# Optimization experiments

Measured on AMD Instinct MI355X. Metric: run time of the kernel, lower is better.

## Reference

```python
import jax, jax.numpy as jnp
import numpy as np

N_NODES = 50000
N_EDGES = 800000
IN_DIM = 64
HID = 64
OUT_DIM = 40
NEG_SLOPE = 0.2


def _gat_layer(x, src, dst, W, b, att, bias, n_nodes):
    # x: [N, Fin] -> lin -> [N, Fout]; heads = 1
    h = x @ W.T + b
    x_i = h[dst]                      # [E, F] target features
    x_j = h[src]                      # [E, F] source features
    # edge attention logits: cat([x_i, x_j]) @ att.T -> [E, 1]
    alpha = jnp.concatenate([x_i, x_j], axis=-1) @ att.T
    alpha = jax.nn.leaky_relu(alpha, NEG_SLOPE)
    # segment softmax over destination node (pyg_utils.softmax)
    amax = jax.ops.segment_max(alpha, dst, num_segments=n_nodes)
    e = jnp.exp(alpha - amax[dst])
    denom = jax.ops.segment_sum(e, dst, num_segments=n_nodes)
    alpha = e / (denom[dst] + 1e-16)
    # message = alpha * x_j, aggr='add' scatter to dst, then + bias
    out = jax.ops.segment_sum(x_j * alpha, dst, num_segments=n_nodes)
    return out + bias


def setup_inputs() -> dict:
    key = jax.random.key(0)
    ks = jax.random.split(key, 12)
    x = jax.random.normal(ks[0], (N_NODES, IN_DIM), dtype=jnp.float32)
    edge_index = jax.random.randint(ks[1], (2, N_EDGES), 0, N_NODES, dtype=jnp.int64)
    def glorot(k, shape):
        fan_in, fan_out = shape[1], shape[0]
        lim = float(np.sqrt(6.0 / (fan_in + fan_out)))
        return jax.random.uniform(k, shape, jnp.float32, -lim, lim)
    W1 = glorot(ks[2], (HID, IN_DIM))
    b1 = jnp.zeros((HID,), jnp.float32)
    att1 = glorot(ks[3], (1, 2 * HID))
    bias1 = jnp.zeros((HID,), jnp.float32)
    W2 = glorot(ks[4], (HID, HID))
    b2 = jnp.zeros((HID,), jnp.float32)
    att2 = glorot(ks[5], (1, 2 * HID))
    bias2 = jnp.zeros((HID,), jnp.float32)
    Wp1 = glorot(ks[6], (HID, HID))
    bp1 = jnp.zeros((HID,), jnp.float32)
    Wp2 = glorot(ks[7], (OUT_DIM, HID))
    bp2 = jnp.zeros((OUT_DIM,), jnp.float32)
    return {"x": x, "edge_index": edge_index,
            "W1": W1, "b1": b1, "att1": att1, "bias1": bias1,
            "W2": W2, "b2": b2, "att2": att2, "bias2": bias2,
            "Wp1": Wp1, "bp1": bp1, "Wp2": Wp2, "bp2": bp2}


def reference(x, edge_index, W1, b1, att1, bias1, W2, b2, att2, bias2,
              Wp1, bp1, Wp2, bp2):
    src, dst = edge_index[0], edge_index[1]
    n = x.shape[0]
    # layer 1 (GAT) + relu; dropout p=0 in eval -> identity
    h = jax.nn.relu(_gat_layer(x, src, dst, W1, b1, att1, bias1, n))
    # layer 2 (GAT) + relu
    h = jax.nn.relu(_gat_layer(h, src, dst, W2, b2, att2, bias2, n))
    # post-MP MLP + log_softmax over classes
    h = h @ Wp1.T + bp1
    logits = h @ Wp2.T + bp2
    return jax.nn.log_softmax(logits, axis=1)
```

## Files before the change

kernel.cpp:

```cpp
#include <hip/hip_runtime.h>
#include <hip/hip_fp16.h>
#include <math.h>

#define NN 50000
#define NE 800000
#define NEG 0.2f

#define NPB 128
#define CHK 6250
#define NBUK 98
#define LCAP 10240

typedef __attribute__((ext_vector_type(8))) short short8v;
typedef __attribute__((ext_vector_type(4))) float f32x4;

__device__ __forceinline__ float lrelu(float x){ return x > 0.f ? x : NEG * x; }

__device__ __forceinline__ float bcastf(float v, int l){
    return __uint_as_float(__builtin_amdgcn_readlane(__float_as_uint(v), l));
}
__device__ __forceinline__ int bcasti(int v, int l){
    return (int)__builtin_amdgcn_readlane((unsigned)v, l);
}
__device__ __forceinline__ short bf16t(float x){ return (short)(__float_as_uint(x) >> 16); }
__device__ __forceinline__ float bf16tof(short s){
    return __uint_as_float(((unsigned)(unsigned short)s) << 16);
}

__global__ __launch_bounds__(256) void k_cntA(const int* __restrict__ dst,
                                              int* __restrict__ counts){
    __shared__ int c[NBUK];
    int tid = threadIdx.x, blk = blockIdx.x;
    for (int i = tid; i < NBUK; i += 256) c[i] = 0;
    __syncthreads();
    int beg = blk * CHK, end = min(beg + CHK, NE);
    for (int i = beg + tid; i < end; i += 256) atomicAdd(&c[dst[i] >> 9], 1);
    __syncthreads();
    for (int i = tid; i < NBUK; i += 256) counts[i * NPB + blk] = c[i];
}

__global__ __launch_bounds__(1024) void k_scanB(int* __restrict__ counts,
                                                int* __restrict__ bbase){
    __shared__ int swave[16];
    int tid = threadIdx.x, lane = tid & 63, wid = tid >> 6;
    const int M = NBUK * NPB;
    int carry = 0;
    for (int base = 0; base < M; base += 1024){
        int i = base + tid;
        int v = (i < M) ? counts[i] : 0;
        int incl = v;
        #pragma unroll
        for (int off = 1; off < 64; off <<= 1){
            int t = __shfl_up(incl, off);
            if (lane >= off) incl += t;
        }
        if (lane == 63) swave[wid] = incl;
        __syncthreads();
        if (wid == 0){
            int sv = (lane < 16) ? swave[lane] : 0;
            #pragma unroll
            for (int off = 1; off < 16; off <<= 1){
                int t = __shfl_up(sv, off);
                if (lane >= off) sv += t;
            }
            if (lane < 16) swave[lane] = sv;
        }
        __syncthreads();
        int woff = wid ? swave[wid - 1] : 0;
        if (i < M) counts[i] = carry + woff + incl - v;
        carry += swave[15];
        __syncthreads();
    }
    for (int i = tid; i < NBUK; i += 1024) bbase[i] = counts[i * NPB];
    if (tid == 0) bbase[NBUK] = NE;
}

__global__ __launch_bounds__(256) void k_partC(const int* __restrict__ src,
                                               const int* __restrict__ dst,
                                               const int* __restrict__ cofs,
                                               unsigned* __restrict__ part){
    __shared__ int lcur[NBUK];
    int tid = threadIdx.x, blk = blockIdx.x;
    for (int i = tid; i < NBUK; i += 256) lcur[i] = cofs[i * NPB + blk];
    __syncthreads();
    int beg = blk * CHK, end = min(beg + CHK, NE);
    for (int i = beg + tid; i < end; i += 256){
        int d = dst[i];
        int pos = atomicAdd(&lcur[d >> 9], 1);
        part[pos] = ((unsigned)(d & 511) << 16) | (unsigned)src[i];
    }
}

__global__ __launch_bounds__(256) void k_buildD(const unsigned* __restrict__ part,
                                                const int* __restrict__ bbase,
                                                int* __restrict__ rowstart,
                                                int* __restrict__ csr){
    __shared__ int hist[512], cur[512];
    __shared__ int csrbuf[LCAP];
    __shared__ int swave[4];
    int tid = threadIdx.x, lane = tid & 63, wid = tid >> 6;
    int b = blockIdx.x;
    int ebeg = bbase[b], eend = bbase[b + 1], cnt = eend - ebeg;

    for (int i = tid; i < 512; i += 256) hist[i] = 0;
    __syncthreads();
    for (int i = tid; i < cnt; i += 256) atomicAdd(&hist[part[ebeg + i] >> 16], 1);
    __syncthreads();

    int h0 = hist[2 * tid], h1 = hist[2 * tid + 1];
    int v = h0 + h1, incl = v;
    #pragma unroll
    for (int off = 1; off < 64; off <<= 1){
        int t = __shfl_up(incl, off);
        if (lane >= off) incl += t;
    }
    if (lane == 63) swave[wid] = incl;
    __syncthreads();
    int woff = 0;
    #pragma unroll
    for (int w = 0; w < 4; ++w) if (w < wid) woff += swave[w];
    int e0 = woff + incl - v;
    int e1 = e0 + h0;
    cur[2 * tid] = e0; cur[2 * tid + 1] = e1;
    int gi = b * 512 + 2 * tid;
    if (gi     <= NN) rowstart[gi]     = ebeg + e0;
    if (gi + 1 <= NN) rowstart[gi + 1] = ebeg + e1;
    __syncthreads();

    for (int i = tid; i < cnt; i += 256){
        unsigned u = part[ebeg + i];
        int lp = atomicAdd(&cur[u >> 16], 1);
        if (lp < LCAP) csrbuf[lp] = (int)(u & 0xFFFFu);
    }
    __syncthreads();
    int m = min(cnt, LCAP);
    for (int i = tid; i < m; i += 256) csr[ebeg + i] = csrbuf[i];
}

__global__ __launch_bounds__(256) void k_lin_mfma(const float* __restrict__ X,
                                                  const float* __restrict__ W,
                                                  const float* __restrict__ b,
                                                  const float* __restrict__ att,
                                                  __half* __restrict__ Hh,
                                                  float* __restrict__ ad,
                                                  float* __restrict__ as_, int n){
    int lane = threadIdx.x & 63, wid = threadIdx.x >> 6;
    int nb = blockIdx.x * 64 + wid * 16;
    if (nb >= n) return;
    int r0 = lane & 15, rg = lane >> 4;

    short8v a_hi[2], a_lo[2];
    int arow = nb + r0; if (arow >= n) arow = n - 1;
    const float* xp = X + (size_t)arow * 64 + rg * 8;
    #pragma unroll
    for (int ks = 0; ks < 2; ++ks){
        #pragma unroll
        for (int j = 0; j < 8; ++j){
            float v = xp[ks * 32 + j];
            short h = bf16t(v);
            a_hi[ks][j] = h;
            a_lo[ks][j] = bf16t(v - bf16tof(h));
        }
    }

    f32x4 acc[4] = {{0,0,0,0},{0,0,0,0},{0,0,0,0},{0,0,0,0}};
    #pragma unroll
    for (int nt = 0; nt < 4; ++nt){
        const float* wp = W + (size_t)(nt * 16 + r0) * 64 + rg * 8;
        #pragma unroll
        for (int ks = 0; ks < 2; ++ks){
            short8v b_hi, b_lo;
            #pragma unroll
            for (int j = 0; j < 8; ++j){
                float v = wp[ks * 32 + j];
                short h = bf16t(v);
                b_hi[j] = h;
                b_lo[j] = bf16t(v - bf16tof(h));
            }
            acc[nt] = __builtin_amdgcn_mfma_f32_16x16x32_bf16(a_hi[ks], b_hi, acc[nt], 0, 0, 0);
            acc[nt] = __builtin_amdgcn_mfma_f32_16x16x32_bf16(a_hi[ks], b_lo, acc[nt], 0, 0, 0);
            acc[nt] = __builtin_amdgcn_mfma_f32_16x16x32_bf16(a_lo[ks], b_hi, acc[nt], 0, 0, 0);
        }
    }

    #pragma unroll
    for (int nt = 0; nt < 4; ++nt){
        float bb = b[nt * 16 + r0];
        #pragma unroll
        for (int q = 0; q < 4; ++q){
            int node = nb + rg * 4 + q;
            float v = acc[nt][q] + bb;
            acc[nt][q] = v;
            if (node < n) Hh[(size_t)node * 64 + nt * 16 + r0] = __float2half(v);
        }
    }

    float attd[4], atts[4];
    #pragma unroll
    for (int nt = 0; nt < 4; ++nt){
        attd[nt] = att[nt * 16 + r0];
        atts[nt] = att[64 + nt * 16 + r0];
    }
    #pragma unroll
    for (int q = 0; q < 4; ++q){
        float pd = 0.f, ps = 0.f;
        #pragma unroll
        for (int nt = 0; nt < 4; ++nt){
            pd = fmaf(attd[nt], acc[nt][q], pd);
            ps = fmaf(atts[nt], acc[nt][q], ps);
        }
        #pragma unroll
        for (int off = 8; off; off >>= 1){
            pd += __shfl_xor(pd, off);
            ps += __shfl_xor(ps, off);
        }
        int node = nb + rg * 4 + q;
        if (r0 == 0 && node < n){ ad[node] = pd; as_[node] = ps; }
    }
}

__global__ __launch_bounds__(256) void k_agg(const __half* __restrict__ Hh,
                                             const float* __restrict__ ad,
                                             const float* __restrict__ as_,
                                             const int* __restrict__ rowstart,
                                             const int* __restrict__ csr,
                                             const float* __restrict__ bias,
                                             float* __restrict__ OUT, int n){
    int tid = threadIdx.x, lane = tid & 63, wid = tid >> 6;
    int node = blockIdx.x * 4 + wid;
    if (node >= n) return;
    int beg = rowstart[node], end = rowstart[node + 1];
    float adn = ad[node];

    float acc = 0.f, denom = 0.f;
    for (int cbeg = beg; cbeg < end; cbeg += 64){
        int k = cbeg + lane;
        int s = (k < end) ? csr[k] : 0;
        float e = (k < end) ? __expf(lrelu(adn + as_[s])) : 0.f;
        float es = e;
        #pragma unroll
        for (int off = 32; off; off >>= 1) es += __shfl_xor(es, off);
        denom += es;
        int cnt = min(64, end - cbeg);
        int j = 0;
        for (; j + 4 <= cnt; j += 4){
            int   sa = bcasti(s, j),     sb = bcasti(s, j + 1);
            int   sc = bcasti(s, j + 2), sd = bcasti(s, j + 3);
            float ea = bcastf(e, j),     eb = bcastf(e, j + 1);
            float ec = bcastf(e, j + 2), ed = bcastf(e, j + 3);
            float ha = __half2float(Hh[(size_t)sa * 64 + lane]);
            float hb = __half2float(Hh[(size_t)sb * 64 + lane]);
            float hc = __half2float(Hh[(size_t)sc * 64 + lane]);
            float hd = __half2float(Hh[(size_t)sd * 64 + lane]);
            acc = fmaf(ea, ha, acc);
            acc = fmaf(eb, hb, acc);
            acc = fmaf(ec, hc, acc);
            acc = fmaf(ed, hd, acc);
        }
        for (; j < cnt; ++j){
            int   sj = bcasti(s, j);
            float ej = bcastf(e, j);
            acc = fmaf(ej, __half2float(Hh[(size_t)sj * 64 + lane]), acc);
        }
    }

    float o = acc / (denom + 1e-16f) + bias[lane];
    OUT[node * 64 + lane] = fmaxf(o, 0.f);
}

__global__ void k_wcomb(const float* __restrict__ Wp1, const float* __restrict__ bp1,
                        const float* __restrict__ Wp2, const float* __restrict__ bp2,
                        float* __restrict__ Wc, float* __restrict__ bc){
    int idx = blockIdx.x * 256 + threadIdx.x;
    if (idx < 40 * 64){
        int c = idx >> 6, k = idx & 63;
        float s = 0.f;
        #pragma unroll 8
        for (int j = 0; j < 64; ++j) s = fmaf(Wp2[c * 64 + j], Wp1[j * 64 + k], s);
        Wc[idx] = s;
    }
    if (idx < 40){
        float s = bp2[idx];
        for (int j = 0; j < 64; ++j) s = fmaf(Wp2[idx * 64 + j], bp1[j], s);
        bc[idx] = s;
    }
}

__global__ __launch_bounds__(256) void k_mlp_mfma(const float* __restrict__ G,
                                                  const float* __restrict__ Wc,
                                                  const float* __restrict__ bc,
                                                  float* __restrict__ out, int n){
    int lane = threadIdx.x & 63, wid = threadIdx.x >> 6;
    int nb = blockIdx.x * 64 + wid * 16;
    if (nb >= n) return;
    int r0 = lane & 15, rg = lane >> 4;

    short8v a_hi[2], a_lo[2];
    int arow = nb + r0; if (arow >= n) arow = n - 1;
    const float* gp = G + (size_t)arow * 64 + rg * 8;
    #pragma unroll
    for (int ks = 0; ks < 2; ++ks){
        #pragma unroll
        for (int j = 0; j < 8; ++j){
            float v = gp[ks * 32 + j];
            short h = bf16t(v);
            a_hi[ks][j] = h;
            a_lo[ks][j] = bf16t(v - bf16tof(h));
        }
    }

    f32x4 acc[3] = {{0,0,0,0},{0,0,0,0},{0,0,0,0}};
    #pragma unroll
    for (int nt = 0; nt < 3; ++nt){
        int f = nt * 16 + r0;
        int fr = (f < 40) ? f : 39;
        const float* wp = Wc + (size_t)fr * 64 + rg * 8;
        #pragma unroll
        for (int ks = 0; ks < 2; ++ks){
            short8v b_hi, b_lo;
            #pragma unroll
            for (int j = 0; j < 8; ++j){
                float v = wp[ks * 32 + j];
                short h = bf16t(v);
                b_hi[j] = h;
                b_lo[j] = bf16t(v - bf16tof(h));
            }
            acc[nt] = __builtin_amdgcn_mfma_f32_16x16x32_bf16(a_hi[ks], b_hi, acc[nt], 0, 0, 0);
            acc[nt] = __builtin_amdgcn_mfma_f32_16x16x32_bf16(a_hi[ks], b_lo, acc[nt], 0, 0, 0);
            acc[nt] = __builtin_amdgcn_mfma_f32_16x16x32_bf16(a_lo[ks], b_hi, acc[nt], 0, 0, 0);
        }
    }

    float bcv[3];
    #pragma unroll
    for (int nt = 0; nt < 3; ++nt){
        int f = nt * 16 + r0;
        bcv[nt] = (f < 40) ? bc[f] : 0.f;
    }

    #pragma unroll
    for (int q = 0; q < 4; ++q){
        int node = nb + rg * 4 + q;
        float l0 = acc[0][q] + bcv[0];
        float l1 = acc[1][q] + bcv[1];
        float l2 = (32 + r0 < 40) ? acc[2][q] + bcv[2] : -INFINITY;
        float m = fmaxf(l0, fmaxf(l1, l2));
        #pragma unroll
        for (int off = 8; off; off >>= 1) m = fmaxf(m, __shfl_xor(m, off));
        float s = __expf(l0 - m) + __expf(l1 - m) + ((32 + r0 < 40) ? __expf(l2 - m) : 0.f);
        #pragma unroll
        for (int off = 8; off; off >>= 1) s += __shfl_xor(s, off);
        float lse = m + __logf(s);
        if (node < n){
            out[(size_t)node * 40 + r0]      = l0 - lse;
            out[(size_t)node * 40 + 16 + r0] = l1 - lse;
            if (32 + r0 < 40) out[(size_t)node * 40 + 32 + r0] = l2 - lse;
        }
    }
}

extern "C" void kernel_launch(void* const* d_in, const int* in_sizes, int n_in,
                              void* d_out, int out_size, void* d_ws, size_t ws_size,
                              hipStream_t stream){
    const float* x     = (const float*)d_in[0];
    const int*   ei    = (const int*)  d_in[1];
    const float* W1    = (const float*)d_in[2];
    const float* b1    = (const float*)d_in[3];
    const float* att1  = (const float*)d_in[4];
    const float* bias1 = (const float*)d_in[5];
    const float* W2    = (const float*)d_in[6];
    const float* b2    = (const float*)d_in[7];
    const float* att2  = (const float*)d_in[8];
    const float* bias2 = (const float*)d_in[9];
    const float* Wp1   = (const float*)d_in[10];
    const float* bp1   = (const float*)d_in[11];
    const float* Wp2   = (const float*)d_in[12];
    const float* bp2   = (const float*)d_in[13];
    float* out = (float*)d_out;

    float*    base     = (float*)d_ws;
    float*    g        = base;
    __half*   hh       = (__half*)(base + 3200000);
    unsigned* part     = (unsigned*)(base + 4800000);
    int*      csr      = (int*)(base + 5600000);
    int*      counts   = (int*)(base + 6400000);
    int*      bbase    = (int*)(base + 6412800);
    int*      rowstart = (int*)(base + 6413000);
    float*    ad       = base + 6463008;
    float*    as_      = base + 6513008;
    float*    Wc       = base + 6563008;
    float*    bc       = base + 6565568;

    const int* srcv = ei;
    const int* dstv = ei + NE;

    k_cntA  <<<NPB, 256, 0, stream>>>(dstv, counts);
    k_wcomb <<<10, 256, 0, stream>>>(Wp1, bp1, Wp2, bp2, Wc, bc);
    k_scanB <<<1, 1024, 0, stream>>>(counts, bbase);
    k_partC <<<NPB, 256, 0, stream>>>(srcv, dstv, counts, part);
    k_buildD<<<NBUK, 256, 0, stream>>>(part, bbase, rowstart, csr);

    int gb = (NN + 63) / 64;
    int nb = (NN + 3) / 4;
    k_lin_mfma<<<gb, 256, 0, stream>>>(x, W1, b1, att1, hh, ad, as_, NN);
    k_agg     <<<nb, 256, 0, stream>>>(hh, ad, as_, rowstart, csr, bias1, g, NN);
    k_lin_mfma<<<gb, 256, 0, stream>>>(g, W2, b2, att2, hh, ad, as_, NN);
    k_agg     <<<nb, 256, 0, stream>>>(hh, ad, as_, rowstart, csr, bias2, g, NN);
    k_mlp_mfma<<<gb, 256, 0, stream>>>(g, Wc, bc, out, NN);
}
```

Before: 165.8 us.

## Pre-split weights into bf16 hi/lo fragments and vectorize aggregation with half2 lanes

```diff
diff --git a/kernel.cpp b/kernel.cpp
--- a/kernel.cpp
+++ b/kernel.cpp
@@ -18,9 +18,6 @@
 
 __device__ __forceinline__ float bcastf(float v, int l){
     return __uint_as_float(__builtin_amdgcn_readlane(__float_as_uint(v), l));
-}
-__device__ __forceinline__ int bcasti(int v, int l){
-    return (int)__builtin_amdgcn_readlane((unsigned)v, l);
 }
 __device__ __forceinline__ short bf16t(float x){ return (short)(__float_as_uint(x) >> 16); }
 __device__ __forceinline__ float bf16tof(short s){
@@ -137,8 +134,70 @@
     for (int i = tid; i < m; i += 256) csr[ebeg + i] = csrbuf[i];
 }
 
+__global__ __launch_bounds__(256) void k_prep(const float* __restrict__ W1,
+                                              const float* __restrict__ W2,
+                                              const float* __restrict__ Wp1,
+                                              const float* __restrict__ bp1,
+                                              const float* __restrict__ Wp2,
+                                              const float* __restrict__ bp2,
+                                              short8v* __restrict__ w1h, short8v* __restrict__ w1l,
+                                              short8v* __restrict__ w2h, short8v* __restrict__ w2l,
+                                              short8v* __restrict__ wch, short8v* __restrict__ wcl,
+                                              float* __restrict__ bc){
+    int tid = threadIdx.x, b = blockIdx.x;
+    if (b < 2){
+        const float* W = b ? W2 : W1;
+        short8v* Wh = b ? w2h : w1h;
+        short8v* Wl = b ? w2l : w1l;
+        for (int p = tid; p < 512; p += 256){
+            int f = p >> 6, lane = p & 63;
+            int nt = f >> 1, ks = f & 1;
+            int r0 = lane & 15, rg = lane >> 4;
+            const float* wp = W + (size_t)(nt * 16 + r0) * 64 + ks * 32 + rg * 8;
+            short8v hi, lo;
+            #pragma unroll
+            for (int j = 0; j < 8; ++j){
+                float v = wp[j];
+                short h = bf16t(v);
+                hi[j] = h; lo[j] = bf16t(v - bf16tof(h));
+            }
+            Wh[p] = hi; Wl[p] = lo;
+        }
+    } else {
+        __shared__ float wc[2560];
+        for (int i = tid; i < 2560; i += 256){
+            int c = i >> 6, k = i & 63;
+            float s = 0.f;
+            #pragma unroll 8
+            for (int j = 0; j < 64; ++j) s = fmaf(Wp2[c * 64 + j], Wp1[j * 64 + k], s);
+            wc[i] = s;
+        }
+        if (tid < 40){
+            float s = bp2[tid];
+            for (int j = 0; j < 64; ++j) s = fmaf(Wp2[tid * 64 + j], bp1[j], s);
+            bc[tid] = s;
+        }
+        __syncthreads();
+        for (int p = tid; p < 384; p += 256){
+            int f = p >> 6, lane = p & 63;
+            int nt = f >> 1, ks = f & 1;
+            int r0 = lane & 15, rg = lane >> 4;
+            int fr = nt * 16 + r0; if (fr > 39) fr = 39;
+            short8v hi, lo;
+            #pragma unroll
+            for (int j = 0; j < 8; ++j){
+                float v = wc[fr * 64 + ks * 32 + rg * 8 + j];
+                short h = bf16t(v);
+                hi[j] = h; lo[j] = bf16t(v - bf16tof(h));
+            }
+            wch[p] = hi; wcl[p] = lo;
+        }
+    }
+}
+
 __global__ __launch_bounds__(256) void k_lin_mfma(const float* __restrict__ X,
-                                                  const float* __restrict__ W,
+                                                  const short8v* __restrict__ Wh,
+                                                  const short8v* __restrict__ Wl,
                                                   const float* __restrict__ b,
                                                   const float* __restrict__ att,
                                                   __half* __restrict__ Hh,
@@ -166,17 +225,10 @@
     f32x4 acc[4] = {{0,0,0,0},{0,0,0,0},{0,0,0,0},{0,0,0,0}};
     #pragma unroll
     for (int nt = 0; nt < 4; ++nt){
-        const float* wp = W + (size_t)(nt * 16 + r0) * 64 + rg * 8;
         #pragma unroll
         for (int ks = 0; ks < 2; ++ks){
-            short8v b_hi, b_lo;
-            #pragma unroll
-            for (int j = 0; j < 8; ++j){
-                float v = wp[ks * 32 + j];
-                short h = bf16t(v);
-                b_hi[j] = h;
-                b_lo[j] = bf16t(v - bf16tof(h));
-            }
+            short8v b_hi = Wh[(nt * 2 + ks) * 64 + lane];
+            short8v b_lo = Wl[(nt * 2 + ks) * 64 + lane];
             acc[nt] = __builtin_amdgcn_mfma_f32_16x16x32_bf16(a_hi[ks], b_hi, acc[nt], 0, 0, 0);
             acc[nt] = __builtin_amdgcn_mfma_f32_16x16x32_bf16(a_hi[ks], b_lo, acc[nt], 0, 0, 0);
             acc[nt] = __builtin_amdgcn_mfma_f32_16x16x32_bf16(a_lo[ks], b_hi, acc[nt], 0, 0, 0);
@@ -219,20 +271,21 @@
     }
 }
 
-__global__ __launch_bounds__(256) void k_agg(const __half* __restrict__ Hh,
+__global__ __launch_bounds__(256) void k_agg(const __half2* __restrict__ H2,
                                              const float* __restrict__ ad,
                                              const float* __restrict__ as_,
                                              const int* __restrict__ rowstart,
                                              const int* __restrict__ csr,
-                                             const float* __restrict__ bias,
-                                             float* __restrict__ OUT, int n){
+                                             const float2* __restrict__ bias2,
+                                             float2* __restrict__ OUT2, int n){
     int tid = threadIdx.x, lane = tid & 63, wid = tid >> 6;
     int node = blockIdx.x * 4 + wid;
     if (node >= n) return;
     int beg = rowstart[node], end = rowstart[node + 1];
     float adn = ad[node];
-
-    float acc = 0.f, denom = 0.f;
+    int half = lane >> 5, hl = lane & 31;
+
+    float accx = 0.f, accy = 0.f, denom = 0.f;
     for (int cbeg = beg; cbeg < end; cbeg += 64){
         int k = cbeg + lane;
         int s = (k < end) ? csr[k] : 0;
@@ -244,50 +297,38 @@
         int cnt = min(64, end - cbeg);
         int j = 0;
         for (; j + 4 <= cnt; j += 4){
-            int   sa = bcasti(s, j),     sb = bcasti(s, j + 1);
-            int   sc = bcasti(s, j + 2), sd = bcasti(s, j + 3);
-            float ea = bcastf(e, j),     eb = bcastf(e, j + 1);
-            float ec = bcastf(e, j + 2), ed = bcastf(e, j + 3);
-            float ha = __half2float(Hh[(size_t)sa * 64 + lane]);
-            float hb = __half2float(Hh[(size_t)sb * 64 + lane]);
-            float hc = __half2float(Hh[(size_t)sc * 64 + lane]);
-            float hd = __half2float(Hh[(size_t)sd * 64 + lane]);
-            acc = fmaf(ea, ha, acc);
-            acc = fmaf(eb, hb, acc);
-            acc = fmaf(ec, hc, acc);
-            acc = fmaf(ed, hd, acc);
-        }
-        for (; j < cnt; ++j){
-            int   sj = bcasti(s, j);
-            float ej = bcastf(e, j);
-            acc = fmaf(ej, __half2float(Hh[(size_t)sj * 64 + lane]), acc);
-        }
-    }
-
-    float o = acc / (denom + 1e-16f) + bias[lane];
-    OUT[node * 64 + lane] = fmaxf(o, 0.f);
-}
-
-__global__ void k_wcomb(const float* __restrict__ Wp1, const float* __restrict__ bp1,
-                        const float* __restrict__ Wp2, const float* __restrict__ bp2,
-                        float* __restrict__ Wc, float* __restrict__ bc){
-    int idx = blockIdx.x * 256 + threadIdx.x;
-    if (idx < 40 * 64){
-        int c = idx >> 6, k = idx & 63;
-        float s = 0.f;
-        #pragma unroll 8
-        for (int j = 0; j < 64; ++j) s = fmaf(Wp2[c * 64 + j], Wp1[j * 64 + k], s);
-        Wc[idx] = s;
-    }
-    if (idx < 40){
-        float s = bp2[idx];
-        for (int j = 0; j < 64; ++j) s = fmaf(Wp2[idx * 64 + j], bp1[j], s);
-        bc[idx] = s;
+            int i0 = j + half, i1 = j + 2 + half;
+            int   s0 = __shfl(s, i0), s1 = __shfl(s, i1);
+            float e0 = __shfl(e, i0), e1 = __shfl(e, i1);
+            __half2 ha = H2[(size_t)s0 * 32 + hl];
+            __half2 hb = H2[(size_t)s1 * 32 + hl];
+            float2 fa = __half22float2(ha), fb = __half22float2(hb);
+            accx = fmaf(e0, fa.x, accx); accy = fmaf(e0, fa.y, accy);
+            accx = fmaf(e1, fb.x, accx); accy = fmaf(e1, fb.y, accy);
+        }
+        for (; j < cnt; j += 2){
+            int idx = j + half;
+            int   se = __shfl(s, idx);
+            float ee = __shfl(e, idx);
+            float2 f = __half22float2(H2[(size_t)se * 32 + hl]);
+            accx = fmaf(ee, f.x, accx); accy = fmaf(ee, f.y, accy);
+        }
+    }
+    accx += __shfl_xor(accx, 32);
+    accy += __shfl_xor(accy, 32);
+    if (half == 0){
+        float2 bb = bias2[hl];
+        float inv = 1.f / (denom + 1e-16f);
+        float2 o;
+        o.x = fmaxf(fmaf(accx, inv, bb.x), 0.f);
+        o.y = fmaxf(fmaf(accy, inv, bb.y), 0.f);
+        OUT2[(size_t)node * 32 + hl] = o;
     }
 }
 
 __global__ __launch_bounds__(256) void k_mlp_mfma(const float* __restrict__ G,
-                                                  const float* __restrict__ Wc,
+                                                  const short8v* __restrict__ Wh,
+                                                  const short8v* __restrict__ Wl,
                                                   const float* __restrict__ bc,
                                                   float* __restrict__ out, int n){
     int lane = threadIdx.x & 63, wid = threadIdx.x >> 6;
@@ -312,19 +353,10 @@
     f32x4 acc[3] = {{0,0,0,0},{0,0,0,0},{0,0,0,0}};
     #pragma unroll
     for (int nt = 0; nt < 3; ++nt){
-        int f = nt * 16 + r0;
-        int fr = (f < 40) ? f : 39;
-        const float* wp = Wc + (size_t)fr * 64 + rg * 8;
         #pragma unroll
         for (int ks = 0; ks < 2; ++ks){
-            short8v b_hi, b_lo;
-            #pragma unroll
-            for (int j = 0; j < 8; ++j){
-                float v = wp[ks * 32 + j];
-                short h = bf16t(v);
-                b_hi[j] = h;
-                b_lo[j] = bf16t(v - bf16tof(h));
-            }
+            short8v b_hi = Wh[(nt * 2 + ks) * 64 + lane];
+            short8v b_lo = Wl[(nt * 2 + ks) * 64 + lane];
             acc[nt] = __builtin_amdgcn_mfma_f32_16x16x32_bf16(a_hi[ks], b_hi, acc[nt], 0, 0, 0);
             acc[nt] = __builtin_amdgcn_mfma_f32_16x16x32_bf16(a_hi[ks], b_lo, acc[nt], 0, 0, 0);
             acc[nt] = __builtin_amdgcn_mfma_f32_16x16x32_bf16(a_lo[ks], b_hi, acc[nt], 0, 0, 0);
@@ -388,23 +420,31 @@
     int*      rowstart = (int*)(base + 6413000);
     float*    ad       = base + 6463008;
     float*    as_      = base + 6513008;
-    float*    Wc       = base + 6563008;
-    float*    bc       = base + 6565568;
+    float*    bc       = base + 6563008;
+    short8v*  w1h      = (short8v*)(base + 6563072);
+    short8v*  w1l      = (short8v*)(base + 6565120);
+    short8v*  w2h      = (short8v*)(base + 6567168);
+    short8v*  w2l      = (short8v*)(base + 6569216);
+    short8v*  wch      = (short8v*)(base + 6571264);
+    short8v*  wcl      = (short8v*)(base + 6572800);
 
     const int* srcv = ei;
     const int* dstv = ei + NE;
 
     k_cntA  <<<NPB, 256, 0, stream>>>(dstv, counts);
-    k_wcomb <<<10, 256, 0, stream>>>(Wp1, bp1, Wp2, bp2, Wc, bc);
+    k_prep  <<<3, 256, 0, stream>>>(W1, W2, Wp1, bp1, Wp2, bp2,
+                                    w1h, w1l, w2h, w2l, wch, wcl, bc);
     k_scanB <<<1, 1024, 0, stream>>>(counts, bbase);
     k_partC <<<NPB, 256, 0, stream>>>(srcv, dstv, counts, part);
     k_buildD<<<NBUK, 256, 0, stream>>>(part, bbase, rowstart, csr);
 
     int gb = (NN + 63) / 64;
     int nb = (NN + 3) / 4;
-    k_lin_mfma<<<gb, 256, 0, stream>>>(x, W1, b1, att1, hh, ad, as_, NN);
-    k_agg     <<<nb, 256, 0, stream>>>(hh, ad, as_, rowstart, csr, bias1, g, NN);
-    k_lin_mfma<<<gb, 256, 0, stream>>>(g, W2, b2, att2, hh, ad, as_, NN);
-    k_agg     <<<nb, 256, 0, stream>>>(hh, ad, as_, rowstart, csr, bias2, g, NN);
-    k_mlp_mfma<<<gb, 256, 0, stream>>>(g, Wc, bc, out, NN);
-}
+    k_lin_mfma<<<gb, 256, 0, stream>>>(x, w1h, w1l, b1, att1, hh, ad, as_, NN);
+    k_agg     <<<nb, 256, 0, stream>>>((const __half2*)hh, ad, as_, rowstart, csr,
+                                       (const float2*)bias1, (float2*)g, NN);
+    k_lin_mfma<<<gb, 256, 0, stream>>>(g, w2h, w2l, b2, att2, hh, ad, as_, NN);
+    k_agg     <<<nb, 256, 0, stream>>>((const __half2*)hh, ad, as_, rowstart, csr,
+                                       (const float2*)bias2, (float2*)g, NN);
+    k_mlp_mfma<<<gb, 256, 0, stream>>>(g, wch, wcl, bc, out, NN);
+}
```

After: 163.3 us. About the same (-1.5%).
